# Kernel optimization log

Hardware: AMD Instinct MI355X
Metric: run time of the kernel (lower is better)

The kernel has to match this reference:

```python
import jax, jax.numpy as jnp
import numpy as np

N = 100000
IN_C = 128
HID = 8
HEADS = 8
OUT_C = 16
NEG_SLOPE = 0.2  # PyG GATConv default leaky_relu slope
EPS = 1e-16


def setup_inputs() -> dict:
    key = jax.random.key(0)
    ks = jax.random.split(key, 10)
    E = 1600000
    x = jax.random.normal(ks[0], (N, IN_C), dtype=jnp.float32)
    edge_index = jax.random.randint(ks[1], (2, E), 0, N, dtype=jnp.int64)
    g = lambda k, shape: jax.random.normal(k, shape, dtype=jnp.float32) * 0.1
    # layer 1: in -> hid, heads=HEADS, concat
    W1 = g(ks[2], (IN_C, HEADS * HID))
    att_src1 = g(ks[3], (HEADS, HID))
    att_dst1 = g(ks[4], (HEADS, HID))
    b1 = jnp.zeros((HEADS * HID,), jnp.float32)
    # layer 2: hid*heads -> out, heads=1, concat=False (mean)
    W2 = g(ks[5], (HEADS * HID, 1 * OUT_C))
    att_src2 = g(ks[6], (1, OUT_C))
    att_dst2 = g(ks[7], (1, OUT_C))
    b2 = jnp.zeros((OUT_C,), jnp.float32)
    return {"x": x, "edge_index": edge_index, "W1": W1, "att_src1": att_src1,
            "att_dst1": att_dst1, "b1": b1, "W2": W2, "att_src2": att_src2,
            "att_dst2": att_dst2, "b2": b2}


def gat_conv(x, src, dst, W, att_src, att_dst, bias, concat):
    # x: [N, F_in]; src/dst: [E] (self-loops already included)
    H, C = att_src.shape
    h = (x @ W).reshape(N, H, C)                      # [N, H, C]
    a_src = jnp.sum(h * att_src, axis=-1)             # [N, H]
    a_dst = jnp.sum(h * att_dst, axis=-1)             # [N, H]
    alpha = a_src[src] + a_dst[dst]                   # [E, H]
    alpha = jax.nn.leaky_relu(alpha, NEG_SLOPE)
    # segment softmax over incoming edges of each destination node
    amax = jax.ops.segment_max(alpha, dst, num_segments=N)
    alpha = jnp.exp(alpha - amax[dst])
    asum = jax.ops.segment_sum(alpha, dst, num_segments=N)
    alpha = alpha / (asum[dst] + EPS)                 # [E, H]
    # (attention dropout skipped: eval mode)
    out = jax.ops.segment_sum(h[src] * alpha[:, :, None], dst, num_segments=N)  # [N, H, C]
    out = out.reshape(N, H * C) if concat else out.mean(axis=1)
    return out + bias


def reference(x, edge_index, W1, att_src1, att_dst1, b1, W2, att_src2, att_dst2, b2):
    # PyG GATConv adds self-loops by default
    loop = jnp.arange(N, dtype=edge_index.dtype)
    src = jnp.concatenate([edge_index[0], loop])
    dst = jnp.concatenate([edge_index[1], loop])
    h = gat_conv(x, src, dst, W1, att_src1, att_dst1, b1, concat=True)
    h = jax.nn.relu(h)
    out = gat_conv(h, src, dst, W2, att_src2, att_dst2, b2, concat=False)
    return jax.nn.relu(out)
```

## Files before the change

kernel.cpp:

```cpp
#include <hip/hip_runtime.h>
#include <hip/hip_fp16.h>

#define IN_C 128
#define NEG 0.2f
#define GAT_EPS 1e-16f
#define NSB_MAX 256
#define SB_SHIFT 9
#define SB_N 512
#define SRC_MASK 0x1FFFF
#define TILE 4096
#define GEMM_BLKS 782
#define CAP_SB 10240
#define CS_STRIDE 72

typedef _Float16 half8 __attribute__((ext_vector_type(8)));
typedef float f32x4 __attribute__((ext_vector_type(4)));

static __device__ inline unsigned f2h(float f) {
    _Float16 h = (_Float16)f;
    unsigned short u;
    __builtin_memcpy(&u, &h, 2);
    return (unsigned)u;
}

__global__ __launch_bounds__(256) void k2_kernel(
    const float* __restrict__ x, const float* __restrict__ W1,
    const float* __restrict__ att_s1, const float* __restrict__ att_d1,
    float* __restrict__ hp, __half* __restrict__ a_src1, float* __restrict__ a_dst1,
    const int* __restrict__ ei, int* __restrict__ sbCnt, unsigned* __restrict__ ebuf,
    int E, int Etot, int NSB, int N, int egrid)
{
    __shared__ __align__(16) char smem[26112];
    int tid = threadIdx.x;

    if ((int)blockIdx.x < egrid) {
        int* lcnt  = (int*)smem;
        int* lbase = lcnt + NSB_MAX;
        for (int i = tid; i < NSB; i += 256) lcnt[i] = 0;
        __syncthreads();
        int base = (int)blockIdx.x * TILE;
        for (int k = tid; k < TILE; k += 256) {
            int e = base + k;
            if (e < Etot) {
                int dst = (e < E) ? ei[E + e] : (e - E);
                atomicAdd(&lcnt[dst >> SB_SHIFT], 1);
            }
        }
        __syncthreads();
        for (int i = tid; i < NSB; i += 256) {
            int c = lcnt[i];
            lbase[i] = c ? (i * CAP_SB + atomicAdd(&sbCnt[i], c)) : 0;
        }
        __syncthreads();
        for (int i = tid; i < NSB; i += 256) lcnt[i] = 0;
        __syncthreads();
        for (int k = tid; k < TILE; k += 256) {
            int e = base + k;
            if (e < Etot) {
                int src, dst;
                if (e < E) { src = ei[e]; dst = ei[E + e]; }
                else       { src = dst = e - E; }
                int b = dst >> SB_SHIFT;
                int r = atomicAdd(&lcnt[b], 1);
                int pos = lbase[b] + r;
                if (pos < (b + 1) * CAP_SB)
                    ebuf[pos] = ((unsigned)(dst & (SB_N - 1)) << 17) | (unsigned)src;
            }
        }
        return;
    }

    _Float16* bfrag = (_Float16*)smem;
    _Float16* csbase = (_Float16*)(smem + 16384);
    float* attS = (float*)(smem + 16384 + 9216);
    float* attD = attS + 64;
    if (tid < 64) { attS[tid] = att_s1[tid]; attD[tid] = att_d1[tid]; }
    for (int idx = tid; idx < 8192; idx += 256) {
        int f = idx >> 9;
        int l = (idx >> 3) & 63;
        int j = idx & 7;
        int k0 = f >> 2, nt = f & 3;
        int row = k0 * 32 + ((l >> 4) << 3) + j;
        int col = (nt << 4) + (l & 15);
        bfrag[idx] = (_Float16)W1[row * 64 + col];
    }
    __syncthreads();

    int lane = tid & 63, wid = tid >> 6;
    _Float16* csw = csbase + wid * (16 * CS_STRIDE);
    int mrow = lane & 15;
    int kgrp = lane >> 4;
    const half8* bf8 = (const half8*)bfrag;
    int ntiles = (N + 15) >> 4;
    int gb = (int)blockIdx.x - egrid;
    for (int t0 = (gb << 3) + (wid << 1); t0 < ntiles; t0 += (GEMM_BLKS << 3)) {
        bool has1 = (t0 + 1) < ntiles;
        int n0 = t0 << 4;
        int arow0 = n0 + mrow;        if (arow0 >= N) arow0 = N - 1;
        int arow1 = n0 + 16 + mrow;   if (arow1 >= N) arow1 = N - 1;
        const float* xr0 = x + (size_t)arow0 * IN_C + (kgrp << 3);
        const float* xr1 = x + (size_t)arow1 * IN_C + (kgrp << 3);
        f32x4 accs[2][4] = {};
        #pragma unroll
        for (int k0 = 0; k0 < 4; ++k0) {
            float4 xa0 = *(const float4*)(xr0 + k0 * 32);
            float4 xb0 = *(const float4*)(xr0 + k0 * 32 + 4);
            float4 xa1 = *(const float4*)(xr1 + k0 * 32);
            float4 xb1 = *(const float4*)(xr1 + k0 * 32 + 4);
            half8 a0, a1;
            a0[0] = (_Float16)xa0.x; a0[1] = (_Float16)xa0.y;
            a0[2] = (_Float16)xa0.z; a0[3] = (_Float16)xa0.w;
            a0[4] = (_Float16)xb0.x; a0[5] = (_Float16)xb0.y;
            a0[6] = (_Float16)xb0.z; a0[7] = (_Float16)xb0.w;
            a1[0] = (_Float16)xa1.x; a1[1] = (_Float16)xa1.y;
            a1[2] = (_Float16)xa1.z; a1[3] = (_Float16)xa1.w;
            a1[4] = (_Float16)xb1.x; a1[5] = (_Float16)xb1.y;
            a1[6] = (_Float16)xb1.z; a1[7] = (_Float16)xb1.w;
            #pragma unroll
            for (int nt = 0; nt < 4; ++nt) {
                accs[0][nt] = __builtin_amdgcn_mfma_f32_16x16x32_f16(a0, bf8[(k0 * 4 + nt) * 64 + lane], accs[0][nt], 0, 0, 0);
                accs[1][nt] = __builtin_amdgcn_mfma_f32_16x16x32_f16(a1, bf8[(k0 * 4 + nt) * 64 + lane], accs[1][nt], 0, 0, 0);
            }
        }
        #pragma unroll
        for (int tt = 0; tt < 2; ++tt) {
            if (tt == 1 && !has1) break;
            int nb0 = n0 + (tt << 4);
            #pragma unroll
            for (int r = 0; r < 4; ++r) {
                int row = (kgrp << 2) + r;
                csw[row * CS_STRIDE +  0 + mrow] = (_Float16)accs[tt][0][r];
                csw[row * CS_STRIDE + 16 + mrow] = (_Float16)accs[tt][1][r];
                csw[row * CS_STRIDE + 32 + mrow] = (_Float16)accs[tt][2][r];
                csw[row * CS_STRIDE + 48 + mrow] = (_Float16)accs[tt][3][r];
            }
            asm volatile("s_waitcnt lgkmcnt(0)" ::: "memory");
            {
                int node = lane >> 2, cq = lane & 3;
                int n = nb0 + node;
                if (n < N) {
                    const int4* src = (const int4*)(csw + node * CS_STRIDE + (cq << 4));
                    int4 v0 = src[0];
                    int4 v1 = src[1];
                    char* dst = (char*)(hp + (size_t)n * 32) + (cq << 5);
                    ((int4*)dst)[0] = v0;
                    ((int4*)dst)[1] = v1;
                }
            }
            #pragma unroll
            for (int pr = 0; pr < 2; ++pr) {
                int node = (pr << 3) + (lane >> 3), head = lane & 7;
                int n = nb0 + node;
                if (n < N) {
                    const half8* hv = (const half8*)(csw + node * CS_STRIDE + (head << 3));
                    half8 v = *hv;
                    float s = 0.f, d = 0.f;
                    #pragma unroll
                    for (int c = 0; c < 8; ++c) {
                        float vv = (float)v[c];
                        s = fmaf(vv, attS[(head << 3) + c], s);
                        d = fmaf(vv, attD[(head << 3) + c], d);
                    }
                    a_src1[n * 8 + head] = __float2half(s);
                    a_dst1[n * 8 + head] = d;
                }
            }
        }
    }
}

__global__ __launch_bounds__(512) void sb_sort_kernel(
    const unsigned* __restrict__ ebuf, const int* __restrict__ sbCnt,
    int2* __restrict__ rowse, int* __restrict__ esrc, int N)
{
    __shared__ int lhist[SB_N];
    __shared__ int lstart[SB_N];
    __shared__ int wsums[8];
    int blk = blockIdx.x, t = threadIdx.x;
    int e0 = blk * CAP_SB;
    int cnt = sbCnt[blk]; if (cnt > CAP_SB) cnt = CAP_SB;
    int e1 = e0 + cnt;
    lhist[t] = 0;
    __syncthreads();
    for (int k = e0 + t; k < e1; k += SB_N)
        atomicAdd(&lhist[ebuf[k] >> 17], 1);
    __syncthreads();
    int lane = t & 63, wv = t >> 6;
    int v = lhist[t];
    int s = v;
    for (int off = 1; off < 64; off <<= 1) {
        int u = __shfl_up(s, off);
        if (lane >= off) s += u;
    }
    if (lane == 63) wsums[wv] = s;
    __syncthreads();
    if (t < 64) {
        int ws = (lane < 8) ? wsums[lane] : 0;
        for (int off = 1; off < 8; off <<= 1) {
            int u = __shfl_up(ws, off);
            if (lane >= off) ws += u;
        }
        if (lane < 8) wsums[lane] = ws;
    }
    __syncthreads();
    int woff = (wv > 0) ? wsums[wv - 1] : 0;
    int excl = woff + s - v;
    lstart[t] = excl;
    int n = (blk << SB_SHIFT) + t;
    if (n < N) rowse[n] = make_int2(e0 + excl, e0 + excl + v);
    __syncthreads();
    lhist[t] = 0;
    __syncthreads();
    for (int k = e0 + t; k < e1; k += SB_N) {
        unsigned pk = ebuf[k];
        int d = pk >> 17;
        int r = atomicAdd(&lhist[d], 1);
        esrc[e0 + lstart[d] + r] = (int)(pk & SRC_MASK);
    }
}

__global__ __launch_bounds__(256) void agg1g2_kernel(
    const int* __restrict__ esrc, const int2* __restrict__ rowse,
    const float* __restrict__ hp, const __half* __restrict__ a_src1,
    const float* __restrict__ a_dst1, const float* __restrict__ b1,
    const float* __restrict__ W2, const float* __restrict__ att_s2,
    const float* __restrict__ att_d2, __half* __restrict__ h2w,
    float* __restrict__ a_src2, float* __restrict__ a_dst2, int N)
{
    __shared__ _Float16 w2frag[1024];
    __shared__ _Float16 h2s[4][16][64];
    __shared__ float cs[4][16 * 20];
    int tid = threadIdx.x;
    for (int idx = tid; idx < 1024; idx += 256) {
        int f = idx >> 9, l = (idx >> 3) & 63, j = idx & 7;
        int row = f * 32 + ((l >> 4) << 3) + j;
        int col = l & 15;
        w2frag[idx] = (_Float16)W2[row * 16 + col];
    }
    __syncthreads();

    int lane = tid & 63, wid = tid >> 6;
    int half = lane >> 5, c2 = lane & 31;
    int h = c2 >> 2;
    int ch = c2 & 7;
    int sbase = half * 32 + h;
    float2 bb = *(const float2*)(b1 + 2 * c2);
    int mrow = lane & 15, kgrp = lane >> 4;
    const half8* w2bf8 = (const half8*)w2frag;
    float* csw = &cs[wid][0];
    int ech = (lane & 3) << 2;
    float as0 = att_s2[ech], as1 = att_s2[ech + 1], as2 = att_s2[ech + 2], as3 = att_s2[ech + 3];
    float ad0 = att_d2[ech], ad1 = att_d2[ech + 1], ad2 = att_d2[ech + 2], ad3 = att_d2[ech + 3];

    int ngroups = (N + 63) >> 6;
    for (int grp = blockIdx.x; grp < ngroups; grp += gridDim.x) {
        int wbase = (grp << 6) + (wid << 4);
        for (int sub = 0; sub < 8; ++sub) {
            int nloc = (sub << 1) + half;
            int n = wbase + nloc;
            bool act = (n < N);
            int nn = act ? n : 0;
            int2 se = rowse[nn];
            int p = se.x;
            int end = act ? se.y : se.x;
            float ad_f = a_dst1[nn * 8 + h];
            float ad_c = a_dst1[nn * 8 + ch];
            float ax = 0.f, ay = 0.f, wsum = 0.f;
            for (; p + 3 < end; p += 4) {
                int s0 = esrc[p], s1 = esrc[p + 1], s2 = esrc[p + 2], s3 = esrc[p + 3];
                int se_ = (c2 & 16) ? ((c2 & 8) ? s3 : s2) : ((c2 & 8) ? s1 : s0);
                float ac = __half2float(a_src1[se_ * 8 + ch]) + ad_c;
                ac = (ac > 0.f) ? ac : NEG * ac;
                float wl = __expf(ac);
                float w0 = __shfl(wl, sbase);
                float w1 = __shfl(wl, sbase + 8);
                float w2 = __shfl(wl, sbase + 16);
                float w3 = __shfl(wl, sbase + 24);
                __half2 q0 = ((const __half2*)(hp + (size_t)s0 * 32))[c2];
                __half2 q1 = ((const __half2*)(hp + (size_t)s1 * 32))[c2];
                __half2 q2 = ((const __half2*)(hp + (size_t)s2 * 32))[c2];
                __half2 q3 = ((const __half2*)(hp + (size_t)s3 * 32))[c2];
                ax = fmaf(w0, __low2float(q0), ax);  ay = fmaf(w0, __high2float(q0), ay);
                ax = fmaf(w1, __low2float(q1), ax);  ay = fmaf(w1, __high2float(q1), ay);
                ax = fmaf(w2, __low2float(q2), ax);  ay = fmaf(w2, __high2float(q2), ay);
                ax = fmaf(w3, __low2float(q3), ax);  ay = fmaf(w3, __high2float(q3), ay);
                wsum += (w0 + w1) + (w2 + w3);
            }
            for (; p < end; ++p) {
                int s0 = esrc[p];
                float a0 = __half2float(a_src1[s0 * 8 + h]) + ad_f;
                __half2 q0 = ((const __half2*)(hp + (size_t)s0 * 32))[c2];
                a0 = (a0 > 0.f) ? a0 : NEG * a0;
                float w0 = __expf(a0);
                ax = fmaf(w0, __low2float(q0), ax);
                ay = fmaf(w0, __high2float(q0), ay);
                wsum += w0;
            }
            float inv = 1.f / (wsum + GAT_EPS);
            float vx = fmaf(ax, inv, bb.x);
            float vy = fmaf(ay, inv, bb.y);
            vx = (act && vx > 0.f) ? vx : 0.f;
            vy = (act && vy > 0.f) ? vy : 0.f;
            ((__half2*)&h2s[wid][nloc][0])[c2] =
                __halves2half2(__float2half(vx), __float2half(vy));
        }
        asm volatile("s_waitcnt lgkmcnt(0)" ::: "memory");
        f32x4 acc = {0, 0, 0, 0};
        const half8* ar = (const half8*)&h2s[wid][mrow][0];
        acc = __builtin_amdgcn_mfma_f32_16x16x32_f16(ar[kgrp], w2bf8[lane], acc, 0, 0, 0);
        acc = __builtin_amdgcn_mfma_f32_16x16x32_f16(ar[4 + kgrp], w2bf8[64 + lane], acc, 0, 0, 0);
        #pragma unroll
        for (int r = 0; r < 4; ++r)
            csw[((kgrp << 2) + r) * 20 + mrow] = acc[r];
        asm volatile("s_waitcnt lgkmcnt(0)" ::: "memory");
        int node = lane >> 2;
        int n = wbase + node;
        if (n < N) {
            float4 v = *(const float4*)&csw[node * 20 + ech];
            unsigned pk0 = f2h(v.x) | (f2h(v.y) << 16);
            unsigned pk1 = f2h(v.z) | (f2h(v.w) << 16);
            *(int2*)((char*)(h2w + (size_t)n * 16) + (ech << 1)) = make_int2((int)pk0, (int)pk1);
            float s = fmaf(v.x, as0, fmaf(v.y, as1, fmaf(v.z, as2, v.w * as3)));
            float d = fmaf(v.x, ad0, fmaf(v.y, ad1, fmaf(v.z, ad2, v.w * ad3)));
            s += __shfl_xor(s, 1); d += __shfl_xor(d, 1);
            s += __shfl_xor(s, 2); d += __shfl_xor(d, 2);
            if ((lane & 3) == 0) { a_src2[n] = s; a_dst2[n] = d; }
        }
    }
}

__global__ __launch_bounds__(256) void agg2_kernel(
    const int* __restrict__ esrc, const int2* __restrict__ rowse,
    const __half* __restrict__ h2w, const float* __restrict__ a_src2,
    const float* __restrict__ a_dst2, const float* __restrict__ b2,
    float* __restrict__ out, int N)
{
    int wslot = (blockIdx.x * 256 + threadIdx.x) >> 6;
    int nw = (gridDim.x * 256) >> 6;
    int lane = threadIdx.x & 63;
    int oct = lane >> 3, c2 = lane & 7;
    for (int base = wslot * 8; base < N; base += nw * 8) {
        int n = base + oct;
        bool act = (n < N);
        int nn = act ? n : 0;
        int2 se = rowse[nn];
        int p = se.x;
        int end = act ? se.y : se.x;
        float ad = a_dst2[nn];
        float ax = 0.f, ay = 0.f, wsum = 0.f;
        for (; p + 3 < end; p += 4) {
            int s0 = esrc[p], s1 = esrc[p + 1], s2 = esrc[p + 2], s3 = esrc[p + 3];
            float a0 = a_src2[s0] + ad;
            float a1 = a_src2[s1] + ad;
            float a2 = a_src2[s2] + ad;
            float a3 = a_src2[s3] + ad;
            __half2 q0 = ((const __half2*)(h2w + (size_t)s0 * 16))[c2];
            __half2 q1 = ((const __half2*)(h2w + (size_t)s1 * 16))[c2];
            __half2 q2 = ((const __half2*)(h2w + (size_t)s2 * 16))[c2];
            __half2 q3 = ((const __half2*)(h2w + (size_t)s3 * 16))[c2];
            a0 = (a0 > 0.f) ? a0 : NEG * a0;
            a1 = (a1 > 0.f) ? a1 : NEG * a1;
            a2 = (a2 > 0.f) ? a2 : NEG * a2;
            a3 = (a3 > 0.f) ? a3 : NEG * a3;
            float w0 = __expf(a0), w1 = __expf(a1), w2 = __expf(a2), w3 = __expf(a3);
            ax = fmaf(w0, __low2float(q0), ax);  ay = fmaf(w0, __high2float(q0), ay);
            ax = fmaf(w1, __low2float(q1), ax);  ay = fmaf(w1, __high2float(q1), ay);
            ax = fmaf(w2, __low2float(q2), ax);  ay = fmaf(w2, __high2float(q2), ay);
            ax = fmaf(w3, __low2float(q3), ax);  ay = fmaf(w3, __high2float(q3), ay);
            wsum += (w0 + w1) + (w2 + w3);
        }
        for (; p < end; ++p) {
            int s0 = esrc[p];
            float a0 = a_src2[s0] + ad;
            __half2 q0 = ((const __half2*)(h2w + (size_t)s0 * 16))[c2];
            a0 = (a0 > 0.f) ? a0 : NEG * a0;
            float w0 = __expf(a0);
            ax = fmaf(w0, __low2float(q0), ax);
            ay = fmaf(w0, __high2float(q0), ay);
            wsum += w0;
        }
        if (act) {
            float inv = 1.f / (wsum + GAT_EPS);
            float2 bb = *(const float2*)(b2 + 2 * c2);
            float2 o;
            o.x = fmaf(ax, inv, bb.x);
            o.y = fmaf(ay, inv, bb.y);
            o.x = o.x > 0.f ? o.x : 0.f;
            o.y = o.y > 0.f ? o.y : 0.f;
            ((float2*)(out + (size_t)n * 16))[c2] = o;
        }
    }
}

extern "C" void kernel_launch(void* const* d_in, const int* in_sizes, int n_in,
                              void* d_out, int out_size, void* d_ws, size_t ws_size,
                              hipStream_t stream)
{
    const float* x      = (const float*)d_in[0];
    const int*   ei     = (const int*)  d_in[1];
    const float* W1     = (const float*)d_in[2];
    const float* att_s1 = (const float*)d_in[3];
    const float* att_d1 = (const float*)d_in[4];
    const float* b1     = (const float*)d_in[5];
    const float* W2     = (const float*)d_in[6];
    const float* att_s2 = (const float*)d_in[7];
    const float* att_d2 = (const float*)d_in[8];
    const float* b2     = (const float*)d_in[9];
    float* out = (float*)d_out;

    int N = in_sizes[0] / IN_C;
    int E = in_sizes[1] / 2;
    int Etot = E + N;
    int NSB = (N + SB_N - 1) >> SB_SHIFT;

    float* ws = (float*)d_ws;
    float*  hp      = ws;
    __half* a_src1  = (__half*)(hp + (size_t)N * 32);
    float*  a_dst1  = (float*)a_src1 + (size_t)N * 4;
    __half* h2w     = (__half*)(a_dst1 + (size_t)N * 8);
    float*  a_src2  = (float*)h2w + (size_t)N * 8;
    float*  a_dst2  = a_src2 + (size_t)N;
    int2* rowse     = (int2*)(a_dst2 + (size_t)N);
    int* sbCnt      = (int*)(rowse + N);
    int* esrc       = sbCnt + NSB_MAX;
    unsigned* ebuf  = (unsigned*)(esrc + (size_t)NSB * CAP_SB);

    int egrid = (Etot + TILE - 1) / TILE;

    hipMemsetAsync(sbCnt, 0, NSB_MAX * sizeof(int), stream);
    k2_kernel<<<egrid + GEMM_BLKS, 256, 0, stream>>>(
        x, W1, att_s1, att_d1, hp, a_src1, a_dst1, ei, sbCnt, ebuf,
        E, Etot, NSB, N, egrid);
    sb_sort_kernel<<<NSB, 512, 0, stream>>>(ebuf, sbCnt, rowse, esrc, N);

    {
        int ngroups = (N + 63) >> 6;
        agg1g2_kernel<<<ngroups, 256, 0, stream>>>(
            esrc, rowse, hp, a_src1, a_dst1, b1,
            W2, att_s2, att_d2, h2w, a_src2, a_dst2, N);
    }
    agg2_kernel<<<1024, 256, 0, stream>>>(esrc, rowse, h2w, a_src2, a_dst2, b2, out, N);
}
```

Measured before the change: 141.7 us.

## Stage x tiles into LDS via async global_load_lds with swizzle, one tile per wave

The GEMM part of k2_kernel now issues async global-to-LDS loads of each wave's 16x128 fp32 x tile into a swizzled shared buffer. These loads overlap with the W1 fragment setup, and the MFMA A operands are then read from LDS instead of straight from global memory. Each wave handles exactly one 16-row tile and the grid is sized to match, instead of a fixed 782 blocks looping over pairs of tiles. Shared memory per block rises to about 49 KB, which may lower occupancy, and the last tile is clamped to overlap the previous rows.

Result: slower. 145.4 us (+2.6%).

```diff
diff --git a/kernel.cpp b/kernel.cpp
--- a/kernel.cpp
+++ b/kernel.cpp
@@ -9,7 +9,6 @@
 #define SB_N 512
 #define SRC_MASK 0x1FFFF
 #define TILE 4096
-#define GEMM_BLKS 782
 #define CAP_SB 10240
 #define CS_STRIDE 72
 
@@ -30,7 +29,7 @@
     const int* __restrict__ ei, int* __restrict__ sbCnt, unsigned* __restrict__ ebuf,
     int E, int Etot, int NSB, int N, int egrid)
 {
-    __shared__ __align__(16) char smem[26112];
+    __shared__ __align__(16) char smem[49664];
     int tid = threadIdx.x;
 
     if ((int)blockIdx.x < egrid) {
@@ -71,9 +70,30 @@
     }
 
     _Float16* bfrag = (_Float16*)smem;
-    _Float16* csbase = (_Float16*)(smem + 16384);
-    float* attS = (float*)(smem + 16384 + 9216);
+    float* attS = (float*)(smem + 16384 + 32768);
     float* attD = attS + 64;
+    int lane = tid & 63, wid = tid >> 6;
+    char* xstage_w = smem + 16384 + wid * 8192;
+
+    int ntiles = (N + 15) >> 4;
+    int gb = (int)blockIdx.x - egrid;
+    int t0 = (gb << 2) + wid;
+    bool havet = (t0 < ntiles);
+    int sbase_row = 0;
+    if (havet) {
+        int n0 = t0 << 4;
+        sbase_row = (n0 + 16 <= N) ? n0 : (N - 16);
+        const char* tb = (const char*)x + (size_t)sbase_row * 512;
+        #pragma unroll
+        for (int i = 0; i < 8; ++i) {
+            int p = i * 1024 + lane * 16;
+            int sp = p ^ (((p >> 9) & 7) << 4);
+            __builtin_amdgcn_global_load_lds(
+                (const __attribute__((address_space(1))) void*)(tb + sp),
+                (__attribute__((address_space(3))) void*)(xstage_w + (i << 10)),
+                16, 0, 0);
+        }
+    }
     if (tid < 64) { attS[tid] = att_s1[tid]; attD[tid] = att_d1[tid]; }
     for (int idx = tid; idx < 8192; idx += 256) {
         int f = idx >> 9;
@@ -86,85 +106,65 @@
     }
     __syncthreads();
 
-    int lane = tid & 63, wid = tid >> 6;
-    _Float16* csw = csbase + wid * (16 * CS_STRIDE);
+    if (!havet) return;
     int mrow = lane & 15;
     int kgrp = lane >> 4;
     const half8* bf8 = (const half8*)bfrag;
-    int ntiles = (N + 15) >> 4;
-    int gb = (int)blockIdx.x - egrid;
-    for (int t0 = (gb << 3) + (wid << 1); t0 < ntiles; t0 += (GEMM_BLKS << 3)) {
-        bool has1 = (t0 + 1) < ntiles;
-        int n0 = t0 << 4;
-        int arow0 = n0 + mrow;        if (arow0 >= N) arow0 = N - 1;
-        int arow1 = n0 + 16 + mrow;   if (arow1 >= N) arow1 = N - 1;
-        const float* xr0 = x + (size_t)arow0 * IN_C + (kgrp << 3);
-        const float* xr1 = x + (size_t)arow1 * IN_C + (kgrp << 3);
-        f32x4 accs[2][4] = {};
+    int swm = (mrow & 7) << 4;
+    f32x4 accs[4] = {};
+    #pragma unroll
+    for (int k0 = 0; k0 < 4; ++k0) {
+        int base = mrow * 512 + (kgrp << 5) + (k0 << 7);
+        int a1 = base ^ swm;
+        float4 xa = *(const float4*)(xstage_w + a1);
+        float4 xb = *(const float4*)(xstage_w + (a1 ^ 16));
+        half8 a;
+        a[0] = (_Float16)xa.x; a[1] = (_Float16)xa.y;
+        a[2] = (_Float16)xa.z; a[3] = (_Float16)xa.w;
+        a[4] = (_Float16)xb.x; a[5] = (_Float16)xb.y;
+        a[6] = (_Float16)xb.z; a[7] = (_Float16)xb.w;
         #pragma unroll
-        for (int k0 = 0; k0 < 4; ++k0) {
-            float4 xa0 = *(const float4*)(xr0 + k0 * 32);
-            float4 xb0 = *(const float4*)(xr0 + k0 * 32 + 4);
-            float4 xa1 = *(const float4*)(xr1 + k0 * 32);
-            float4 xb1 = *(const float4*)(xr1 + k0 * 32 + 4);
-            half8 a0, a1;
-            a0[0] = (_Float16)xa0.x; a0[1] = (_Float16)xa0.y;
-            a0[2] = (_Float16)xa0.z; a0[3] = (_Float16)xa0.w;
-            a0[4] = (_Float16)xb0.x; a0[5] = (_Float16)xb0.y;
-            a0[6] = (_Float16)xb0.z; a0[7] = (_Float16)xb0.w;
-            a1[0] = (_Float16)xa1.x; a1[1] = (_Float16)xa1.y;
-            a1[2] = (_Float16)xa1.z; a1[3] = (_Float16)xa1.w;
-            a1[4] = (_Float16)xb1.x; a1[5] = (_Float16)xb1.y;
-            a1[6] = (_Float16)xb1.z; a1[7] = (_Float16)xb1.w;
+        for (int nt = 0; nt < 4; ++nt)
+            accs[nt] = __builtin_amdgcn_mfma_f32_16x16x32_f16(a, bf8[(k0 * 4 + nt) * 64 + lane], accs[nt], 0, 0, 0);
+    }
+    _Float16* csw = (_Float16*)xstage_w;
+    #pragma unroll
+    for (int r = 0; r < 4; ++r) {
+        int row = (kgrp << 2) + r;
+        csw[row * CS_STRIDE +  0 + mrow] = (_Float16)accs[0][r];
+        csw[row * CS_STRIDE + 16 + mrow] = (_Float16)accs[1][r];
+        csw[row * CS_STRIDE + 32 + mrow] = (_Float16)accs[2][r];
+        csw[row * CS_STRIDE + 48 + mrow] = (_Float16)accs[3][r];
+    }
+    asm volatile("s_waitcnt lgkmcnt(0)" ::: "memory");
+    {
+        int node = lane >> 2, cq = lane & 3;
+        int n = sbase_row + node;
+        if (n < N) {
+            const int4* src = (const int4*)(csw + node * CS_STRIDE + (cq << 4));
+            int4 v0 = src[0];
+            int4 v1 = src[1];
+            char* dst = (char*)(hp + (size_t)n * 32) + (cq << 5);
+            ((int4*)dst)[0] = v0;
+            ((int4*)dst)[1] = v1;
+        }
+    }
+    #pragma unroll
+    for (int pr = 0; pr < 2; ++pr) {
+        int node = (pr << 3) + (lane >> 3), head = lane & 7;
+        int n = sbase_row + node;
+        if (n < N) {
+            const half8* hv = (const half8*)(csw + node * CS_STRIDE + (head << 3));
+            half8 v = *hv;
+            float s = 0.f, d = 0.f;
             #pragma unroll
-            for (int nt = 0; nt < 4; ++nt) {
-                accs[0][nt] = __builtin_amdgcn_mfma_f32_16x16x32_f16(a0, bf8[(k0 * 4 + nt) * 64 + lane], accs[0][nt], 0, 0, 0);
-                accs[1][nt] = __builtin_amdgcn_mfma_f32_16x16x32_f16(a1, bf8[(k0 * 4 + nt) * 64 + lane], accs[1][nt], 0, 0, 0);
+            for (int c = 0; c < 8; ++c) {
+                float vv = (float)v[c];
+                s = fmaf(vv, attS[(head << 3) + c], s);
+                d = fmaf(vv, attD[(head << 3) + c], d);
             }
-        }
-        #pragma unroll
-        for (int tt = 0; tt < 2; ++tt) {
-            if (tt == 1 && !has1) break;
-            int nb0 = n0 + (tt << 4);
-            #pragma unroll
-            for (int r = 0; r < 4; ++r) {
-                int row = (kgrp << 2) + r;
-                csw[row * CS_STRIDE +  0 + mrow] = (_Float16)accs[tt][0][r];
-                csw[row * CS_STRIDE + 16 + mrow] = (_Float16)accs[tt][1][r];
-                csw[row * CS_STRIDE + 32 + mrow] = (_Float16)accs[tt][2][r];
-                csw[row * CS_STRIDE + 48 + mrow] = (_Float16)accs[tt][3][r];
-            }
-            asm volatile("s_waitcnt lgkmcnt(0)" ::: "memory");
-            {
-                int node = lane >> 2, cq = lane & 3;
-                int n = nb0 + node;
-                if (n < N) {
-                    const int4* src = (const int4*)(csw + node * CS_STRIDE + (cq << 4));
-                    int4 v0 = src[0];
-                    int4 v1 = src[1];
-                    char* dst = (char*)(hp + (size_t)n * 32) + (cq << 5);
-                    ((int4*)dst)[0] = v0;
-                    ((int4*)dst)[1] = v1;
-                }
-            }
-            #pragma unroll
-            for (int pr = 0; pr < 2; ++pr) {
-                int node = (pr << 3) + (lane >> 3), head = lane & 7;
-                int n = nb0 + node;
-                if (n < N) {
-                    const half8* hv = (const half8*)(csw + node * CS_STRIDE + (head << 3));
-                    half8 v = *hv;
-                    float s = 0.f, d = 0.f;
-                    #pragma unroll
-                    for (int c = 0; c < 8; ++c) {
-                        float vv = (float)v[c];
-                        s = fmaf(vv, attS[(head << 3) + c], s);
-                        d = fmaf(vv, attD[(head << 3) + c], d);
-                    }
-                    a_src1[n * 8 + head] = __float2half(s);
-                    a_dst1[n * 8 + head] = d;
-                }
-            }
+            a_src1[n * 8 + head] = __float2half(s);
+            a_dst1[n * 8 + head] = d;
         }
     }
 }
@@ -426,9 +426,11 @@
     unsigned* ebuf  = (unsigned*)(esrc + (size_t)NSB * CAP_SB);
 
     int egrid = (Etot + TILE - 1) / TILE;
+    int ntiles = (N + 15) >> 4;
+    int gblks = (ntiles + 3) >> 2;
 
     hipMemsetAsync(sbCnt, 0, NSB_MAX * sizeof(int), stream);
-    k2_kernel<<<egrid + GEMM_BLKS, 256, 0, stream>>>(
+    k2_kernel<<<egrid + gblks, 256, 0, stream>>>(
         x, W1, att_s1, att_d1, hp, a_src1, a_dst1, ei, sbCnt, ebuf,
         E, Etot, NSB, N, egrid);
     sb_sort_kernel<<<NSB, 512, 0, stream>>>(ebuf, sbCnt, rowse, esrc, N);
```
